# Performance work log

Hardware: AMD Instinct MI355X
Metric: run time of the kernel (lower is better)

## Reference

```python
import jax, jax.numpy as jnp
import numpy as np

DIM = 256      # in_channels == hidden_channels
INNER = 256    # heads * dim_head
HEADS = 4
DH = 64        # dim_head = hidden_channels // num_heads
EDGE_DIM = 512 # 2 * in_channels
FF = 1024      # 4 * dim ff expansion
DEPTH = 2
OUT = 1
N = 50000      # two stacked graphs of 25000 nodes
E = 100000
HALF = 25000


def setup_inputs() -> dict:
    key = jax.random.key(0)
    ks = iter(jax.random.split(key, 32))

    def lin(fan_in, fan_out):
        w = jax.random.normal(next(ks), (DEPTH, fan_in, fan_out), jnp.float32) * (1.0 / np.sqrt(fan_in))
        b = jnp.zeros((DEPTH, fan_out), jnp.float32)
        return w, b

    x = jax.random.normal(next(ks), (N, DIM), jnp.float32)
    edge_index = jax.random.randint(next(ks), (2, E), 0, HALF, dtype=jnp.int32)
    Wq, bq = lin(DIM, INNER)
    Wkv, bkv = lin(DIM, 2 * INNER)
    We, be = lin(EDGE_DIM, INNER)
    Wo, bo = lin(INNER, DIM)
    W1, b1 = lin(DIM, FF)
    W2, b2 = lin(FF, DIM)
    g_attn = jax.random.normal(next(ks), (DEPTH, 3 * DIM, 1), jnp.float32) * (1.0 / np.sqrt(3 * DIM))
    g_ff = jax.random.normal(next(ks), (DEPTH, 3 * DIM, 1), jnp.float32) * (1.0 / np.sqrt(3 * DIM))
    ln1_g = jnp.ones((DEPTH, DIM), jnp.float32); ln1_b = jnp.zeros((DEPTH, DIM), jnp.float32)
    ln2_g = jnp.ones((DEPTH, DIM), jnp.float32); ln2_b = jnp.zeros((DEPTH, DIM), jnp.float32)
    Wout = jax.random.normal(next(ks), (DIM, OUT), jnp.float32) * (1.0 / np.sqrt(DIM))
    bout = jnp.zeros((OUT,), jnp.float32)
    return dict(x=x, edge_index=edge_index, ln1_g=ln1_g, ln1_b=ln1_b, Wq=Wq, bq=bq,
                Wkv=Wkv, bkv=bkv, We=We, be=be, Wo=Wo, bo=bo, g_attn=g_attn,
                ln2_g=ln2_g, ln2_b=ln2_b, W1=W1, b1=b1, W2=W2, b2=b2, g_ff=g_ff,
                Wout=Wout, bout=bout)


def _layer_norm(x, g, b):
    mu = jnp.mean(x, axis=-1, keepdims=True)
    var = jnp.mean(jnp.square(x - mu), axis=-1, keepdims=True)
    return (x - mu) * jax.lax.rsqrt(var + 1e-5) * g + b


def _gated_residual(x, res, w):
    # gate = sigmoid(Linear_no_bias(cat(x, res, x - res)))
    gate = jax.nn.sigmoid(jnp.concatenate([x, res, x - res], axis=-1) @ w)  # [n,1]
    return x * gate + res * (1.0 - gate)


def _forward(x, edge_index, ln1_g, ln1_b, Wq, bq, Wkv, bkv, We, be, Wo, bo, g_attn,
             ln2_g, ln2_b, W1, b1, W2, b2, g_ff, Wout, bout):
    src, dst = edge_index[0], edge_index[1]
    # edge_attr = cat(x[src], x[dst]) as built in DeepGraphTransformer_mse.forward
    edge_attr = jnp.concatenate([x[src], x[dst]], axis=-1)  # [E, 2*DIM]
    nodes = x
    n = nodes.shape[0]
    scale = DH ** -0.5
    for l in range(DEPTH):
        xn = _layer_norm(nodes, ln1_g[l], ln1_b[l])
        q = xn @ Wq[l] + bq[l]                                   # [n, INNER]
        k, v = jnp.split(xn @ Wkv[l] + bkv[l], 2, axis=-1)       # [n, INNER] each
        e = edge_attr @ We[l] + be[l]                            # [E, INNER]
        qe = q[dst].reshape(-1, HEADS, DH)                       # [E,H,Dh]
        ke = (k[src] + e).reshape(-1, HEADS, DH)
        ve = (v[src] + e).reshape(-1, HEADS, DH)
        sim = jnp.einsum('ehd,ehd->eh', qe, ke) * scale          # [E,H]
        smax = jax.ops.segment_max(sim, dst, num_segments=n)     # [n,H] (-inf for empty)
        ez = jnp.exp(sim - smax[dst])
        denom = jax.ops.segment_sum(ez, dst, num_segments=n)
        attn = ez / denom[dst]                                   # softmax over incoming edges
        agg = jax.ops.segment_sum(attn[:, :, None] * ve, dst, num_segments=n)
        attn_out = agg.reshape(n, INNER) @ Wo[l] + bo[l]         # [n, DIM]
        nodes = _gated_residual(attn_out, nodes, g_attn[l])
        xn2 = _layer_norm(nodes, ln2_g[l], ln2_b[l])
        h = jax.nn.gelu(xn2 @ W1[l] + b1[l], approximate=False) @ W2[l] + b2[l]
        nodes = _gated_residual(h, nodes, g_ff[l])
    z = nodes @ Wout + bout                                      # [n, OUT]
    return z


def reference(x, edge_index, ln1_g, ln1_b, Wq, bq, Wkv, bkv, We, be, Wo, bo, g_attn,
              ln2_g, ln2_b, W1, b1, W2, b2, g_ff, Wout, bout):
    z = _forward(x, edge_index, ln1_g, ln1_b, Wq, bq, Wkv, bkv, We, be, Wo, bo, g_attn,
                 ln2_g, ln2_b, W1, b1, W2, b2, g_ff, Wout, bout)
    half = z.shape[0] // 2
    z_old, z_new = z[:half], z[half:]
    return (z_new.reshape(-1), z_old, z_new)
```

## Files before the change

kernel.cpp:

```cpp
#include <hip/hip_runtime.h>
#include <cmath>

#define N_NODES 50000
#define N_EDGES 100000
#define HALF_N  25000
#define DIM     256
#define NDEPTH  2
#define MAXDEG  64

#define WT_QKVE 0
#define WT_WO   393216
#define WT_W1   524288
#define WT_W2   786432
#define WT_LAYER 1048576

typedef __bf16 bf16;
typedef bf16 bf16x8 __attribute__((ext_vector_type(8)));
typedef bf16 bf16x4 __attribute__((ext_vector_type(4)));
typedef float f32x4 __attribute__((ext_vector_type(4)));

__device__ __forceinline__ void lds_barrier() {
  asm volatile("s_waitcnt lgkmcnt(0)" ::: "memory");
  __builtin_amdgcn_s_barrier();
  __builtin_amdgcn_sched_barrier(0);
}

__device__ __forceinline__ float wave_sum(float v) {
  v += __shfl_xor(v, 1);
  v += __shfl_xor(v, 2);
  v += __shfl_xor(v, 4);
  v += __shfl_xor(v, 8);
  v += __shfl_xor(v, 16);
  v += __shfl_xor(v, 32);
  return v;
}

__device__ __forceinline__ float fast_gelu(float v) {
  float ax = fabsf(v) * 0.70710678118654752f;
  float t = __builtin_amdgcn_rcpf(fmaf(0.3275911f, ax, 1.0f));
  float p = t * fmaf(t, fmaf(t, fmaf(t, fmaf(t, 1.061405429f, -1.453152027f),
                                     1.421413741f), -0.284496736f), 0.254829592f);
  float e = __expf(-ax * ax);
  float erfv = fmaf(-p, e, 1.0f);
  float ph = copysignf(erfv, v);
  return 0.5f * v * (1.0f + ph);
}

__global__ void ln0_kernel(const float* __restrict__ in, const float* __restrict__ g,
                           const float* __restrict__ b, bf16* __restrict__ A2) {
  int row = blockIdx.x * 4 + (threadIdx.x >> 6);
  if (row >= HALF_N) return;
  int lane = threadIdx.x & 63;
  float4 x = reinterpret_cast<const float4*>(in + (size_t)row * DIM)[lane];
  float mu = wave_sum(x.x + x.y + x.z + x.w) * (1.0f / DIM);
  float d0 = x.x - mu, d1 = x.y - mu, d2 = x.z - mu, d3 = x.w - mu;
  float var = wave_sum(d0*d0 + d1*d1 + d2*d2 + d3*d3) * (1.0f / DIM);
  float r = rsqrtf(var + 1e-5f);
  float4 gv = reinterpret_cast<const float4*>(g)[lane];
  float4 bv = reinterpret_cast<const float4*>(b)[lane];
  bf16x4 o;
  o[0] = (bf16)(d0 * r * gv.x + bv.x);
  o[1] = (bf16)(d1 * r * gv.y + bv.y);
  o[2] = (bf16)(d2 * r * gv.z + bv.z);
  o[3] = (bf16)(d3 * r * gv.w + bv.w);
  *reinterpret_cast<bf16x4*>(A2 + (size_t)row * 512 + lane * 4) = o;
}

template<int KK, int NJ>
__global__ __launch_bounds__(256, 2) void gemm_nloop(
    const bf16* __restrict__ A, const bf16* __restrict__ Wp,
    const float* __restrict__ bias, bf16* __restrict__ C, int M) {
  constexpr int STEPS = KK / 64;
  __shared__ bf16x8 As[KK * 8];
  __shared__ bf16 Cs[64 * 128];
  const int tid = threadIdx.x;
  const int lane = tid & 63, wv = tid >> 6;
  const int lm = lane & 15, kb = (lane >> 4) & 3;
  const int row0 = blockIdx.x * 64;
#pragma unroll
  for (int i = 0; i < KK / 32; ++i) {
    int idx = tid + i * 256;
    int row = idx & 63, k8 = idx >> 6;
    int rga = row0 + row; if (rga >= M) rga = M - 1;
    As[idx] = *reinterpret_cast<const bf16x8*>(A + (size_t)rga * KK + k8 * 8);
  }
  const bf16x8* wb = reinterpret_cast<const bf16x8*>(Wp) + kb * 128 + wv * 32 + lm;
  bf16x8 pfr[2];
#pragma unroll
  for (int ni = 0; ni < 2; ++ni) pfr[ni] = wb[ni * 16];
  lds_barrier();
  for (int jn = 0; jn < NJ; ++jn) {
    f32x4 acc[4][2] = {};
#pragma unroll
    for (int st = 0; st < STEPS; ++st) {
#pragma unroll
      for (int ks = 0; ks < 2; ++ks) {
        bf16x8 bfr[2], af[4];
        if (st == 0 && ks == 0) {
          bfr[0] = pfr[0]; bfr[1] = pfr[1];
        } else {
#pragma unroll
          for (int ni = 0; ni < 2; ++ni)
            bfr[ni] = wb[(size_t)jn * (KK * 16) + st * 1024 + ks * 512 + ni * 16];
        }
#pragma unroll
        for (int mi = 0; mi < 4; ++mi)
          af[mi] = As[(st * 8 + ks * 4 + kb) * 64 + mi * 16 + lm];
#pragma unroll
        for (int mi = 0; mi < 4; ++mi)
#pragma unroll
          for (int ni = 0; ni < 2; ++ni)
            acc[mi][ni] = __builtin_amdgcn_mfma_f32_16x16x32_bf16(af[mi], bfr[ni], acc[mi][ni], 0, 0, 0);
      }
    }
    if (jn + 1 < NJ) {
#pragma unroll
      for (int ni = 0; ni < 2; ++ni)
        pfr[ni] = wb[(size_t)(jn + 1) * (KK * 16) + ni * 16];
    }
    lds_barrier();
#pragma unroll
    for (int ni = 0; ni < 2; ++ni) {
      int c = wv * 32 + ni * 16 + lm;
      float bval = bias[jn * 128 + c];
#pragma unroll
      for (int mi = 0; mi < 4; ++mi)
#pragma unroll
        for (int e = 0; e < 4; ++e) {
          int r = mi * 16 + kb * 4 + e;
          Cs[r * 128 + c] = (bf16)(acc[mi][ni][e] + bval);
        }
    }
    lds_barrier();
    bf16x8* C8 = reinterpret_cast<bf16x8*>(C);
    const bf16x8* Cs8 = (const bf16x8*)Cs;
#pragma unroll
    for (int i = 0; i < 4; ++i) {
      int idx = tid + i * 256;
      int row = idx >> 4, c8 = idx & 15;
      int grow = row0 + row;
      if (grow < M) C8[(size_t)grow * (NJ * 16) + jn * 16 + c8] = Cs8[row * 16 + c8];
    }
  }
}

__global__ __launch_bounds__(256, 2) void wo_fused(
    const bf16* __restrict__ agg, const bf16* __restrict__ A2,
    const bf16* __restrict__ Wp, const float* __restrict__ bvec,
    const float* __restrict__ bo, const int* __restrict__ deg,
    const float* __restrict__ gattn, const float* __restrict__ ln2g,
    const float* __restrict__ ln2b, float* __restrict__ nodes,
    bf16* __restrict__ xn, int rows) {
  __shared__ bf16x8 As[2048];
  __shared__ bf16 Cs[64 * 256];
  const int tid = threadIdx.x;
  const int lane = tid & 63, wv = tid >> 6;
  const int row0 = blockIdx.x * 64;
  if (row0 < HALF_N) {
    const int wr = wv >> 1, wc = wv & 1;
    const int lm = lane & 15, kb = (lane >> 4) & 3;
#pragma unroll
    for (int i = 0; i < 8; ++i) {
      int idx = tid + i * 256;
      int row = idx & 63, k8 = idx >> 6;
      int rga = row0 + row; if (rga >= HALF_N) rga = HALF_N - 1;
      As[idx] = *reinterpret_cast<const bf16x8*>(agg + (size_t)rga * 256 + k8 * 8);
    }
    bf16x8 afx[2][8];
#pragma unroll
    for (int mi = 0; mi < 2; ++mi) {
      int row = row0 + wr * 32 + mi * 16 + lm;
      if (row >= HALF_N) row = HALF_N - 1;
      const bf16* pa = A2 + (size_t)row * 512 + 256 + kb * 8;
#pragma unroll
      for (int t = 0; t < 8; ++t)
        afx[mi][t] = *reinterpret_cast<const bf16x8*>(pa + t * 32);
    }
    lds_barrier();
    const bf16x8* wb = reinterpret_cast<const bf16x8*>(Wp) + kb * 128 + wc * 64 + lm;
    for (int jn = 0; jn < 2; ++jn) {
      f32x4 acc[2][4] = {};
#pragma unroll
      for (int st = 0; st < 8; ++st) {
#pragma unroll
        for (int ks = 0; ks < 2; ++ks) {
          bf16x8 bfr[4], af[2];
#pragma unroll
          for (int ni = 0; ni < 4; ++ni)
            bfr[ni] = wb[jn * 8192 + (st * 8 + ks * 4) * 128 + ni * 16];
#pragma unroll
          for (int mi = 0; mi < 2; ++mi)
            af[mi] = (st < 4) ? As[(st * 8 + ks * 4 + kb) * 64 + wr * 32 + mi * 16 + lm]
                              : afx[mi][(st - 4) * 2 + ks];
#pragma unroll
          for (int mi = 0; mi < 2; ++mi)
#pragma unroll
            for (int ni = 0; ni < 4; ++ni)
              acc[mi][ni] = __builtin_amdgcn_mfma_f32_16x16x32_bf16(af[mi], bfr[ni], acc[mi][ni], 0, 0, 0);
        }
      }
#pragma unroll
      for (int ni = 0; ni < 4; ++ni) {
        int cfull = jn * 128 + wc * 64 + ni * 16 + lm;
        float bval = bvec[cfull];
#pragma unroll
        for (int mi = 0; mi < 2; ++mi)
#pragma unroll
          for (int e = 0; e < 4; ++e) {
            int r = wr * 32 + mi * 16 + kb * 4 + e;
            int ch = (cfull >> 3) ^ (r & 7);
            Cs[r * 256 + ch * 8 + (cfull & 7)] = (bf16)(acc[mi][ni][e] + bval);
          }
      }
    }
    lds_barrier();
    for (int pass = 0; pass < 16; ++pass) {
      int r = pass * 4 + wv;
      int grow = row0 + r;
      float x0, x1, x2, x3;
      if (grow >= HALF_N || deg[grow] == 0) {
        float4 bo4 = reinterpret_cast<const float4*>(bo)[lane];
        x0 = bo4.x; x1 = bo4.y; x2 = bo4.z; x3 = bo4.w;
      } else {
        int ch = (lane >> 1) ^ (r & 7);
        bf16x4 c4 = *reinterpret_cast<const bf16x4*>(Cs + r * 256 + ch * 8 + (lane & 1) * 4);
        x0 = (float)c4[0]; x1 = (float)c4[1]; x2 = (float)c4[2]; x3 = (float)c4[3];
      }
      float4 rv = reinterpret_cast<const float4*>(nodes + (size_t)grow * 256)[lane];
      float4 w0 = reinterpret_cast<const float4*>(gattn)[lane];
      float4 w1 = reinterpret_cast<const float4*>(gattn + 256)[lane];
      float4 w2 = reinterpret_cast<const float4*>(gattn + 512)[lane];
      float dot = x0 * (w0.x + w2.x) + rv.x * (w1.x - w2.x)
                + x1 * (w0.y + w2.y) + rv.y * (w1.y - w2.y)
                + x2 * (w0.z + w2.z) + rv.z * (w1.z - w2.z)
                + x3 * (w0.w + w2.w) + rv.w * (w1.w - w2.w);
      dot = wave_sum(dot);
      float gate = 1.0f / (1.0f + __expf(-dot));
      float n0 = fmaf(x0 - rv.x, gate, rv.x);
      float n1 = fmaf(x1 - rv.y, gate, rv.y);
      float n2 = fmaf(x2 - rv.z, gate, rv.z);
      float n3 = fmaf(x3 - rv.w, gate, rv.w);
      float4 o; o.x = n0; o.y = n1; o.z = n2; o.w = n3;
      reinterpret_cast<float4*>(nodes + (size_t)grow * 256)[lane] = o;
      float mu = wave_sum(n0 + n1 + n2 + n3) * (1.0f / DIM);
      float d0 = n0 - mu, d1 = n1 - mu, d2 = n2 - mu, d3 = n3 - mu;
      float var = wave_sum(d0*d0 + d1*d1 + d2*d2 + d3*d3) * (1.0f / DIM);
      float rs = rsqrtf(var + 1e-5f);
      float4 gv = reinterpret_cast<const float4*>(ln2g)[lane];
      float4 bv = reinterpret_cast<const float4*>(ln2b)[lane];
      bf16x4 ob;
      ob[0] = (bf16)(d0 * rs * gv.x + bv.x);
      ob[1] = (bf16)(d1 * rs * gv.y + bv.y);
      ob[2] = (bf16)(d2 * rs * gv.z + bv.z);
      ob[3] = (bf16)(d3 * rs * gv.w + bv.w);
      *reinterpret_cast<bf16x4*>(xn + (size_t)grow * 256 + lane * 4) = ob;
    }
  } else {
    float4 bo4 = reinterpret_cast<const float4*>(bo)[lane];
    for (int pass = 0; pass < 16; ++pass) {
      int grow = row0 + pass * 4 + wv;
      if (grow >= rows) continue;
      float x0 = bo4.x, x1 = bo4.y, x2 = bo4.z, x3 = bo4.w;
      float4 rv = reinterpret_cast<const float4*>(nodes + (size_t)grow * 256)[lane];
      float4 w0 = reinterpret_cast<const float4*>(gattn)[lane];
      float4 w1 = reinterpret_cast<const float4*>(gattn + 256)[lane];
      float4 w2 = reinterpret_cast<const float4*>(gattn + 512)[lane];
      float dot = x0 * (w0.x + w2.x) + rv.x * (w1.x - w2.x)
                + x1 * (w0.y + w2.y) + rv.y * (w1.y - w2.y)
                + x2 * (w0.z + w2.z) + rv.z * (w1.z - w2.z)
                + x3 * (w0.w + w2.w) + rv.w * (w1.w - w2.w);
      dot = wave_sum(dot);
      float gate = 1.0f / (1.0f + __expf(-dot));
      float n0 = fmaf(x0 - rv.x, gate, rv.x);
      float n1 = fmaf(x1 - rv.y, gate, rv.y);
      float n2 = fmaf(x2 - rv.z, gate, rv.z);
      float n3 = fmaf(x3 - rv.w, gate, rv.w);
      float4 o; o.x = n0; o.y = n1; o.z = n2; o.w = n3;
      reinterpret_cast<float4*>(nodes + (size_t)grow * 256)[lane] = o;
      float mu = wave_sum(n0 + n1 + n2 + n3) * (1.0f / DIM);
      float d0 = n0 - mu, d1 = n1 - mu, d2 = n2 - mu, d3 = n3 - mu;
      float var = wave_sum(d0*d0 + d1*d1 + d2*d2 + d3*d3) * (1.0f / DIM);
      float rs = rsqrtf(var + 1e-5f);
      float4 gv = reinterpret_cast<const float4*>(ln2g)[lane];
      float4 bv = reinterpret_cast<const float4*>(ln2b)[lane];
      bf16x4 ob;
      ob[0] = (bf16)(d0 * rs * gv.x + bv.x);
      ob[1] = (bf16)(d1 * rs * gv.y + bv.y);
      ob[2] = (bf16)(d2 * rs * gv.z + bv.z);
      ob[3] = (bf16)(d3 * rs * gv.w + bv.w);
      *reinterpret_cast<bf16x4*>(xn + (size_t)grow * 256 + lane * 4) = ob;
    }
  }
}

template<int LAST>
__global__ __launch_bounds__(512, 4) void ff_fused(
    const bf16* __restrict__ A, const bf16* __restrict__ W1p,
    const float* __restrict__ b1, const bf16* __restrict__ W2p,
    const float* __restrict__ b2, float* __restrict__ nodes,
    const float* __restrict__ gff, const float* __restrict__ ln1g,
    const float* __restrict__ ln1b, bf16* __restrict__ A2,
    const float* __restrict__ Wout, const float* __restrict__ bout,
    float* __restrict__ out, int M) {
  __shared__ char smem[65536];
  bf16x8* Xs = (bf16x8*)smem;
  bf16*   Cs = (bf16*)smem;
  bf16x8* Hs = (bf16x8*)(smem + 32768);
  const int tid = threadIdx.x;
  const int lane = tid & 63, wv = tid >> 6;
  const int lm = lane & 15, kb = (lane >> 4) & 3;
  const int row0 = blockIdx.x * 64;
#pragma unroll
  for (int i = 0; i < 4; ++i) {
    int idx = tid + i * 512;
    int row = idx & 63, k8 = idx >> 6;
    int rga = row0 + row; if (rga >= M) rga = M - 1;
    Xs[idx] = *reinterpret_cast<const bf16x8*>(A + (size_t)rga * 256 + k8 * 8);
  }
  lds_barrier();
  const bf16x8* w1b = (const bf16x8*)W1p + kb * 128 + wv * 16 + lm;
  const bf16x8* w2b = (const bf16x8*)W2p + kb * 256 + wv * 32 + lm;
  f32x4 acc[4][2] = {};
  for (int j = 0; j < 8; ++j) {
    bf16x8 pf2[4];
#pragma unroll
    for (int ks = 0; ks < 2; ++ks)
#pragma unroll
      for (int ni = 0; ni < 2; ++ni)
        pf2[ks * 2 + ni] = w2b[j * 4096 + ks * 1024 + ni * 16];
    f32x4 acc1[4] = {};
#pragma unroll
    for (int half = 0; half < 2; ++half) {
#pragma unroll
      for (int ks = 0; ks < 4; ++ks) {
        bf16x8 bfr = w1b[j * 4096 + half * 2048 + ks * 512];
        bf16x8 af[4];
#pragma unroll
        for (int mi = 0; mi < 4; ++mi)
          af[mi] = Xs[(half * 16 + ks * 4 + kb) * 64 + mi * 16 + lm];
#pragma unroll
        for (int mi = 0; mi < 4; ++mi)
          acc1[mi] = __builtin_amdgcn_mfma_f32_16x16x32_bf16(af[mi], bfr, acc1[mi], 0, 0, 0);
      }
    }
    {
      bf16* hsb = (bf16*)(Hs + (j & 1) * 1024);
      int c = wv * 16 + lm;
      float bval = b1[j * 128 + c];
#pragma unroll
      for (int mi = 0; mi < 4; ++mi)
#pragma unroll
        for (int e = 0; e < 4; ++e) {
          int r = mi * 16 + kb * 4 + e;
          float v = fast_gelu(acc1[mi][e] + bval);
          hsb[((c >> 3) * 64 + r) * 8 + (c & 7)] = (bf16)v;
        }
    }
    lds_barrier();
    const bf16x8* hb = Hs + (j & 1) * 1024;
#pragma unroll
    for (int h2 = 0; h2 < 2; ++h2) {
#pragma unroll
      for (int ks = 0; ks < 2; ++ks) {
        bf16x8 bfr[2], af[4];
#pragma unroll
        for (int ni = 0; ni < 2; ++ni)
          bfr[ni] = (h2 == 0) ? pf2[ks * 2 + ni]
                              : w2b[j * 4096 + 2048 + ks * 1024 + ni * 16];
#pragma unroll
        for (int mi = 0; mi < 4; ++mi)
          af[mi] = hb[(h2 * 8 + ks * 4 + kb) * 64 + mi * 16 + lm];
#pragma unroll
        for (int mi = 0; mi < 4; ++mi)
#pragma unroll
          for (int ni = 0; ni < 2; ++ni)
            acc[mi][ni] = __builtin_amdgcn_mfma_f32_16x16x32_bf16(af[mi], bfr[ni], acc[mi][ni], 0, 0, 0);
      }
    }
  }
#pragma unroll
  for (int ni = 0; ni < 2; ++ni) {
    int c = wv * 32 + ni * 16 + lm;
    float bval = b2[c];
#pragma unroll
    for (int mi = 0; mi < 4; ++mi)
#pragma unroll
      for (int e = 0; e < 4; ++e) {
        int r = mi * 16 + kb * 4 + e;
        int ch = (c >> 3) ^ (r & 7);
        Cs[r * 256 + ch * 8 + (c & 7)] = (bf16)(acc[mi][ni][e] + bval);
      }
  }
  lds_barrier();
  for (int pass = 0; pass < 8; ++pass) {
    int r = pass * 8 + wv;
    int grow = row0 + r;
    if (grow >= M) continue;
    int ch = (lane >> 1) ^ (r & 7);
    bf16x4 c4 = *reinterpret_cast<const bf16x4*>(Cs + r * 256 + ch * 8 + (lane & 1) * 4);
    float x0 = (float)c4[0], x1 = (float)c4[1], x2 = (float)c4[2], x3 = (float)c4[3];
    float4 rv = reinterpret_cast<const float4*>(nodes + (size_t)grow * 256)[lane];
    float4 w0 = reinterpret_cast<const float4*>(gff)[lane];
    float4 w1 = reinterpret_cast<const float4*>(gff + 256)[lane];
    float4 w2 = reinterpret_cast<const float4*>(gff + 512)[lane];
    float dot = x0 * (w0.x + w2.x) + rv.x * (w1.x - w2.x)
              + x1 * (w0.y + w2.y) + rv.y * (w1.y - w2.y)
              + x2 * (w0.z + w2.z) + rv.z * (w1.z - w2.z)
              + x3 * (w0.w + w2.w) + rv.w * (w1.w - w2.w);
    dot = wave_sum(dot);
    float gate = 1.0f / (1.0f + __expf(-dot));
    float n0 = fmaf(x0 - rv.x, gate, rv.x);
    float n1 = fmaf(x1 - rv.y, gate, rv.y);
    float n2 = fmaf(x2 - rv.z, gate, rv.z);
    float n3 = fmaf(x3 - rv.w, gate, rv.w);
    if (LAST) {
      float4 wo4 = reinterpret_cast<const float4*>(Wout)[lane];
      float z = n0 * wo4.x + n1 * wo4.y + n2 * wo4.z + n3 * wo4.w;
      z = wave_sum(z);
      if (lane == 0) {
        z += bout[0];
        if (grow < HALF_N) {
          out[HALF_N + grow] = z;
        } else {
          int jj = grow - HALF_N;
          out[jj] = z;
          out[2 * HALF_N + jj] = z;
        }
      }
    } else {
      float4 o; o.x = n0; o.y = n1; o.z = n2; o.w = n3;
      reinterpret_cast<float4*>(nodes + (size_t)grow * 256)[lane] = o;
      if (grow < HALF_N) {
        float mu = wave_sum(n0 + n1 + n2 + n3) * (1.0f / DIM);
        float d0 = n0 - mu, d1 = n1 - mu, d2 = n2 - mu, d3 = n3 - mu;
        float var = wave_sum(d0*d0 + d1*d1 + d2*d2 + d3*d3) * (1.0f / DIM);
        float rs = rsqrtf(var + 1e-5f);
        float4 gv = reinterpret_cast<const float4*>(ln1g)[lane];
        float4 bv = reinterpret_cast<const float4*>(ln1b)[lane];
        bf16x4 ob;
        ob[0] = (bf16)(d0 * rs * gv.x + bv.x);
        ob[1] = (bf16)(d1 * rs * gv.y + bv.y);
        ob[2] = (bf16)(d2 * rs * gv.z + bv.z);
        ob[3] = (bf16)(d3 * rs * gv.w + bv.w);
        *reinterpret_cast<bf16x4*>(A2 + (size_t)grow * 512 + lane * 4) = ob;
      }
    }
  }
}

__global__ void ell_build(const int* __restrict__ ei, int* __restrict__ deg,
                          int* __restrict__ ell) {
  int e = blockIdx.x * 256 + threadIdx.x;
  if (e >= N_EDGES) return;
  int s = ei[e], d = ei[N_EDGES + e];
  int pos = atomicAdd(&deg[d], 1);
  if (pos < MAXDEG) ell[d * MAXDEG + pos] = s;
}

__global__ void attn_gather(const int* __restrict__ deg, const int* __restrict__ ell,
                            const bf16* __restrict__ qkv, bf16* __restrict__ agg) {
  int d = blockIdx.x * 4 + (threadIdx.x >> 6);
  if (d >= HALF_N) return;
  int lane = threadIdx.x & 63;
  int cnt = deg[d]; if (cnt > MAXDEG) cnt = MAXDEG;
  const bf16* qr = qkv + (size_t)d * 768;
  bf16x4 qb = *reinterpret_cast<const bf16x4*>(qr + lane * 4);
  float q0 = (float)qb[0], q1 = (float)qb[1], q2 = (float)qb[2], q3 = (float)qb[3];
  float m = -INFINITY, den = 0.0f, a0 = 0.0f, a1 = 0.0f, a2 = 0.0f, a3 = 0.0f;
  int i = 0;
  for (; i + 2 <= cnt; i += 2) {
    int s0 = ell[d * MAXDEG + i];
    int s1 = ell[d * MAXDEG + i + 1];
    bf16x8 k0 = *reinterpret_cast<const bf16x8*>(qkv + (size_t)s0 * 768 + 256 + lane * 8);
    bf16x8 k1 = *reinterpret_cast<const bf16x8*>(qkv + (size_t)s1 * 768 + 256 + lane * 8);
    float p0 = q0 * (float)k0[0] + q1 * (float)k0[1] + q2 * (float)k0[2] + q3 * (float)k0[3];
    float p1 = q0 * (float)k1[0] + q1 * (float)k1[1] + q2 * (float)k1[2] + q3 * (float)k1[3];
    p0 += __shfl_xor(p0, 1); p1 += __shfl_xor(p1, 1);
    p0 += __shfl_xor(p0, 2); p1 += __shfl_xor(p1, 2);
    p0 += __shfl_xor(p0, 4); p1 += __shfl_xor(p1, 4);
    p0 += __shfl_xor(p0, 8); p1 += __shfl_xor(p1, 8);
    float s0v = p0 * 0.125f, s1v = p1 * 0.125f;
    float nm = fmaxf(m, fmaxf(s0v, s1v));
    float sc = __expf(m - nm);
    float w0 = __expf(s0v - nm), w1 = __expf(s1v - nm);
    den = den * sc + w0 + w1;
    a0 = a0 * sc + w0 * (float)k0[4] + w1 * (float)k1[4];
    a1 = a1 * sc + w0 * (float)k0[5] + w1 * (float)k1[5];
    a2 = a2 * sc + w0 * (float)k0[6] + w1 * (float)k1[6];
    a3 = a3 * sc + w0 * (float)k0[7] + w1 * (float)k1[7];
    m = nm;
  }
  if (i < cnt) {
    int s = ell[d * MAXDEG + i];
    bf16x8 kv8 = *reinterpret_cast<const bf16x8*>(qkv + (size_t)s * 768 + 256 + lane * 8);
    float p = q0 * (float)kv8[0] + q1 * (float)kv8[1] + q2 * (float)kv8[2] + q3 * (float)kv8[3];
    p += __shfl_xor(p, 1); p += __shfl_xor(p, 2);
    p += __shfl_xor(p, 4); p += __shfl_xor(p, 8);
    float sim = p * 0.125f;
    float nm = fmaxf(m, sim);
    float sc = __expf(m - nm);
    float w = __expf(sim - nm);
    den = den * sc + w;
    a0 = a0 * sc + w * (float)kv8[4];
    a1 = a1 * sc + w * (float)kv8[5];
    a2 = a2 * sc + w * (float)kv8[6];
    a3 = a3 * sc + w * (float)kv8[7];
    m = nm;
  }
  bf16x4 o;
  if (cnt > 0) {
    float inv = 1.0f / den;
    o[0] = (bf16)(a0 * inv);
    o[1] = (bf16)(a1 * inv);
    o[2] = (bf16)(a2 * inv);
    o[3] = (bf16)(a3 * inv);
  } else {
    o[0] = (bf16)0.0f; o[1] = (bf16)0.0f; o[2] = (bf16)0.0f; o[3] = (bf16)0.0f;
  }
  *reinterpret_cast<bf16x4*>(agg + (size_t)d * DIM + lane * 4) = o;
}

__global__ void prep_w(const float* __restrict__ Wq, const float* __restrict__ Wkv,
                       const float* __restrict__ We, const float* __restrict__ Wo,
                       const float* __restrict__ W1, const float* __restrict__ W2,
                       bf16* __restrict__ wt) {
  int idx = blockIdx.x * 256 + threadIdx.x;
  if (idx >= 2 * WT_LAYER) return;
  int l = idx / WT_LAYER, r = idx % WT_LAYER;
  float v;
  if (r < 393216) {
    int jn = r >> 16, t = r & 65535;
    int k8 = t >> 10, u = t & 1023, n = u >> 3, e = u & 7;
    int ncol = jn * 128 + n, k = k8 * 8 + e;
    if (ncol < 256) {
      v = (k < 256) ? Wq[l * 65536 + k * 256 + ncol] : 0.0f;
    } else {
      int u2 = ncol - 256;
      int c = (u2 >> 3) * 4 + (u2 & 3);
      int half = (u2 >> 2) & 1;
      if (k < 256) v = Wkv[l * 131072 + k * 512 + half * 256 + c];
      else         v = We[l * 131072 + (k - 256) * 256 + c];
    }
  } else if (r < 524288) {
    int rr = r - 393216;
    int jn = rr >> 16, t = rr & 65535;
    int k8 = t >> 10, u = t & 1023, n = u >> 3, e = u & 7;
    int k = k8 * 8 + e;
    if (k >= 256) return;
    v = Wo[l * 65536 + k * 256 + jn * 128 + n];
  } else if (r < 786432) {
    int rr = r - 524288;
    int j = rr >> 15, t = rr & 32767;
    int k8 = t >> 10, u = t & 1023, n = u >> 3, e = u & 7;
    v = W1[l * 262144 + (k8 * 8 + e) * 1024 + j * 128 + n];
  } else {
    int rr = r - 786432;
    int j = rr >> 15, t = rr & 32767;
    int k8 = t >> 11, u = t & 2047, n = u >> 3, e = u & 7;
    v = W2[l * 262144 + (j * 128 + k8 * 8 + e) * 256 + n];
  }
  wt[idx] = (bf16)v;
}

__global__ void prep_weff(const float* __restrict__ We, const float* __restrict__ Wo,
                          bf16* __restrict__ wt) {
  int idx = blockIdx.x * 256 + threadIdx.x;
  if (idx >= 2 * 65536) return;
  int l = idx >> 16, r = idx & 65535;
  int k = r >> 8, n = r & 255;
  const float* wer = We + l * 131072 + (256 + k) * 256;
  const float* wor = Wo + l * 65536 + n;
  float acc = 0.0f;
#pragma unroll 4
  for (int m = 0; m < 256; ++m) acc += wer[m] * wor[m * 256];
  int kf = 256 + k;
  size_t off = (size_t)l * WT_LAYER + WT_WO +
               (n >> 7) * 65536 + (kf >> 3) * 1024 + (n & 127) * 8 + (kf & 7);
  wt[off] = (bf16)acc;
}

__global__ void prep_bvec(const float* __restrict__ be, const float* __restrict__ Wo,
                          const float* __restrict__ bo, float* __restrict__ biasq) {
  int idx = blockIdx.x * 256 + threadIdx.x;
  if (idx >= 512) return;
  int l = idx >> 8, n = idx & 255;
  const float* ber = be + l * 256;
  const float* wor = Wo + l * 65536 + n;
  float acc = bo[l * 256 + n];
#pragma unroll 4
  for (int m = 0; m < 256; ++m) acc += ber[m] * wor[m * 256];
  biasq[1536 + l * 256 + n] = acc;
}

__global__ void prep_bias(const float* __restrict__ bq, const float* __restrict__ bkv,
                          float* __restrict__ biasq) {
  int i = blockIdx.x * 256 + threadIdx.x;
  if (i >= 1536) return;
  int l = i / 768, n = i % 768;
  float v;
  if (n < 256) v = bq[l * 256 + n];
  else {
    int u2 = n - 256;
    int c = (u2 >> 3) * 4 + (u2 & 3);
    int half = (u2 >> 2) & 1;
    v = bkv[l * 512 + half * 256 + c];
  }
  biasq[i] = v;
}

__global__ void prep_x(const float* __restrict__ x, bf16* __restrict__ A2) {
  int i = blockIdx.x * 256 + threadIdx.x;
  if (i >= HALF_N * 64) return;
  int row = i >> 6, c = i & 63;
  float4 v = reinterpret_cast<const float4*>(x)[i];
  bf16x4 o;
  o[0] = (bf16)v.x; o[1] = (bf16)v.y; o[2] = (bf16)v.z; o[3] = (bf16)v.w;
  *reinterpret_cast<bf16x4*>(A2 + (size_t)row * 512 + 256 + c * 4) = o;
}

extern "C" void kernel_launch(void* const* d_in, const int* in_sizes, int n_in,
                              void* d_out, int out_size, void* d_ws, size_t ws_size,
                              hipStream_t stream) {
  const float* x     = (const float*)d_in[0];
  const int*   ei    = (const int*)d_in[1];
  const float* ln1_g = (const float*)d_in[2];
  const float* ln1_b = (const float*)d_in[3];
  const float* Wq    = (const float*)d_in[4];
  const float* bq    = (const float*)d_in[5];
  const float* Wkv   = (const float*)d_in[6];
  const float* bkv   = (const float*)d_in[7];
  const float* We    = (const float*)d_in[8];
  const float* be    = (const float*)d_in[9];
  const float* Wo    = (const float*)d_in[10];
  const float* bo    = (const float*)d_in[11];
  const float* g_attn= (const float*)d_in[12];
  const float* ln2_g = (const float*)d_in[13];
  const float* ln2_b = (const float*)d_in[14];
  const float* W1    = (const float*)d_in[15];
  const float* b1    = (const float*)d_in[16];
  const float* W2    = (const float*)d_in[17];
  const float* b2    = (const float*)d_in[18];
  const float* g_ff  = (const float*)d_in[19];
  const float* Wout  = (const float*)d_in[20];
  const float* bout  = (const float*)d_in[21];
  float* out = (float*)d_out;

  char* base = (char*)d_ws;
  float* nodes   = (float*)base;  base += (size_t)N_NODES * DIM * 4;
  bf16*  A2      = (bf16*)base;   base += (size_t)HALF_N * 512 * 2;
  bf16*  xn_bf   = (bf16*)base;   base += (size_t)N_NODES * DIM * 2;
  bf16*  qkv     = (bf16*)base;   base += (size_t)HALF_N * 768 * 2;
  bf16*  agg     = (bf16*)base;   base += (size_t)HALF_N * DIM * 2;
  bf16*  wt      = (bf16*)base;   base += (size_t)2 * WT_LAYER * 2;
  float* biasq   = (float*)base;  base += 2048 * 4;
  int*   deg     = (int*)base;    base += HALF_N * 4;
  int*   ell     = (int*)base;    base += (size_t)HALF_N * MAXDEG * 4;

  hipMemcpyAsync(nodes, x, (size_t)N_NODES * DIM * sizeof(float),
                 hipMemcpyDeviceToDevice, stream);
  prep_w<<<(2 * WT_LAYER + 255) / 256, 256, 0, stream>>>(Wq, Wkv, We, Wo, W1, W2, wt);
  prep_weff<<<(2 * 65536 + 255) / 256, 256, 0, stream>>>(We, Wo, wt);
  prep_bvec<<<2, 256, 0, stream>>>(be, Wo, bo, biasq);
  prep_bias<<<6, 256, 0, stream>>>(bq, bkv, biasq);
  prep_x<<<(HALF_N * 64 + 255) / 256, 256, 0, stream>>>(x, A2);
  hipMemsetAsync(deg, 0, HALF_N * sizeof(int), stream);
  ell_build<<<(N_EDGES + 255) / 256, 256, 0, stream>>>(ei, deg, ell);

  const int GP_H = (HALF_N + 63) / 64;
  const int GP_N = (N_NODES + 63) / 64;

  for (int l = 0; l < NDEPTH; ++l) {
    const bf16* wl = wt + (size_t)l * WT_LAYER;
    if (l == 0)
      ln0_kernel<<<(HALF_N + 3) / 4, 256, 0, stream>>>(x, ln1_g, ln1_b, A2);
    gemm_nloop<512, 6><<<GP_H, 256, 0, stream>>>(A2, wl + WT_QKVE, biasq + l * 768, qkv, HALF_N);
    attn_gather<<<(HALF_N + 3) / 4, 256, 0, stream>>>(deg, ell, qkv, agg);
    wo_fused<<<GP_N, 256, 0, stream>>>(agg, A2, wl + WT_WO, biasq + 1536 + l * 256,
                                       bo + l * DIM, deg, g_attn + l * 768,
                                       ln2_g + l * DIM, ln2_b + l * DIM,
                                       nodes, xn_bf, N_NODES);
    if (l < NDEPTH - 1) {
      ff_fused<0><<<GP_N, 512, 0, stream>>>(
          xn_bf, wl + WT_W1, b1 + l * 1024, wl + WT_W2, b2 + l * DIM,
          nodes, g_ff + l * 768, ln1_g + (l + 1) * DIM, ln1_b + (l + 1) * DIM, A2,
          nullptr, nullptr, nullptr, N_NODES);
    } else {
      ff_fused<1><<<GP_N, 512, 0, stream>>>(
          xn_bf, wl + WT_W1, b1 + l * 1024, wl + WT_W2, b2 + l * DIM,
          nodes, g_ff + l * 768, nullptr, nullptr, nullptr,
          Wout, bout, out, N_NODES);
    }
  }
}
```

Before: 499.7 us.

## Approximate GELU with exp2 sigmoid, widen QKV GEMM to 512 threads, hoist params

Replaces the erf-polynomial GELU with a cheaper sigmoid-form approximation based on one exp2 and one reciprocal. The QKV GEMM block is doubled to 8 waves, each computing a single 16-column tile, for more parallelism per block. Gate weights, LayerNorm parameters and Wout are loaded once per thread, outside the row loops, in the fused kernels. The GELU approximation changes numerics relative to exact erf GELU and may affect accuracy.

```diff
diff --git a/kernel.cpp b/kernel.cpp
--- a/kernel.cpp
+++ b/kernel.cpp
@@ -35,15 +35,11 @@
   return v;
 }
 
-__device__ __forceinline__ float fast_gelu(float v) {
-  float ax = fabsf(v) * 0.70710678118654752f;
-  float t = __builtin_amdgcn_rcpf(fmaf(0.3275911f, ax, 1.0f));
-  float p = t * fmaf(t, fmaf(t, fmaf(t, fmaf(t, 1.061405429f, -1.453152027f),
-                                     1.421413741f), -0.284496736f), 0.254829592f);
-  float e = __expf(-ax * ax);
-  float erfv = fmaf(-p, e, 1.0f);
-  float ph = copysignf(erfv, v);
-  return 0.5f * v * (1.0f + ph);
+__device__ __forceinline__ float fast_gelu(float x) {
+  float p = x * x;
+  float q = fmaf(p, -0.10294437f, -2.3022112f);
+  float e = exp2f(x * q);
+  return x * __builtin_amdgcn_rcpf(1.0f + e);
 }
 
 __global__ void ln0_kernel(const float* __restrict__ in, const float* __restrict__ g,
@@ -67,7 +63,7 @@
 }
 
 template<int KK, int NJ>
-__global__ __launch_bounds__(256, 2) void gemm_nloop(
+__global__ __launch_bounds__(512, 2) void gemm_nloop(
     const bf16* __restrict__ A, const bf16* __restrict__ Wp,
     const float* __restrict__ bias, bf16* __restrict__ C, int M) {
   constexpr int STEPS = KK / 64;
@@ -78,65 +74,52 @@
   const int lm = lane & 15, kb = (lane >> 4) & 3;
   const int row0 = blockIdx.x * 64;
 #pragma unroll
-  for (int i = 0; i < KK / 32; ++i) {
-    int idx = tid + i * 256;
+  for (int i = 0; i < KK / 64; ++i) {
+    int idx = tid + i * 512;
     int row = idx & 63, k8 = idx >> 6;
     int rga = row0 + row; if (rga >= M) rga = M - 1;
     As[idx] = *reinterpret_cast<const bf16x8*>(A + (size_t)rga * KK + k8 * 8);
   }
-  const bf16x8* wb = reinterpret_cast<const bf16x8*>(Wp) + kb * 128 + wv * 32 + lm;
-  bf16x8 pfr[2];
-#pragma unroll
-  for (int ni = 0; ni < 2; ++ni) pfr[ni] = wb[ni * 16];
+  const bf16x8* wb = reinterpret_cast<const bf16x8*>(Wp) + kb * 128 + wv * 16 + lm;
+  bf16x8 pfr = wb[0];
   lds_barrier();
   for (int jn = 0; jn < NJ; ++jn) {
-    f32x4 acc[4][2] = {};
+    f32x4 acc[4] = {};
 #pragma unroll
     for (int st = 0; st < STEPS; ++st) {
 #pragma unroll
       for (int ks = 0; ks < 2; ++ks) {
-        bf16x8 bfr[2], af[4];
-        if (st == 0 && ks == 0) {
-          bfr[0] = pfr[0]; bfr[1] = pfr[1];
-        } else {
-#pragma unroll
-          for (int ni = 0; ni < 2; ++ni)
-            bfr[ni] = wb[(size_t)jn * (KK * 16) + st * 1024 + ks * 512 + ni * 16];
-        }
+        bf16x8 bfr = (st == 0 && ks == 0)
+                   ? pfr
+                   : wb[(size_t)jn * (KK * 16) + st * 1024 + ks * 512];
+        bf16x8 af[4];
 #pragma unroll
         for (int mi = 0; mi < 4; ++mi)
           af[mi] = As[(st * 8 + ks * 4 + kb) * 64 + mi * 16 + lm];
 #pragma unroll
         for (int mi = 0; mi < 4; ++mi)
-#pragma unroll
-          for (int ni = 0; ni < 2; ++ni)
-            acc[mi][ni] = __builtin_amdgcn_mfma_f32_16x16x32_bf16(af[mi], bfr[ni], acc[mi][ni], 0, 0, 0);
-      }
-    }
-    if (jn + 1 < NJ) {
-#pragma unroll
-      for (int ni = 0; ni < 2; ++ni)
-        pfr[ni] = wb[(size_t)(jn + 1) * (KK * 16) + ni * 16];
-    }
+          acc[mi] = __builtin_amdgcn_mfma_f32_16x16x32_bf16(af[mi], bfr, acc[mi], 0, 0, 0);
+      }
+    }
+    if (jn + 1 < NJ) pfr = wb[(size_t)(jn + 1) * (KK * 16)];
     lds_barrier();
-#pragma unroll
-    for (int ni = 0; ni < 2; ++ni) {
-      int c = wv * 32 + ni * 16 + lm;
+    {
+      int c = wv * 16 + lm;
       float bval = bias[jn * 128 + c];
 #pragma unroll
       for (int mi = 0; mi < 4; ++mi)
 #pragma unroll
         for (int e = 0; e < 4; ++e) {
           int r = mi * 16 + kb * 4 + e;
-          Cs[r * 128 + c] = (bf16)(acc[mi][ni][e] + bval);
+          Cs[r * 128 + c] = (bf16)(acc[mi][e] + bval);
         }
     }
     lds_barrier();
     bf16x8* C8 = reinterpret_cast<bf16x8*>(C);
     const bf16x8* Cs8 = (const bf16x8*)Cs;
 #pragma unroll
-    for (int i = 0; i < 4; ++i) {
-      int idx = tid + i * 256;
+    for (int i = 0; i < 2; ++i) {
+      int idx = tid + i * 512;
       int row = idx >> 4, c8 = idx & 15;
       int grow = row0 + row;
       if (grow < M) C8[(size_t)grow * (NJ * 16) + jn * 16 + c8] = Cs8[row * 16 + c8];
@@ -156,6 +139,14 @@
   const int tid = threadIdx.x;
   const int lane = tid & 63, wv = tid >> 6;
   const int row0 = blockIdx.x * 64;
+  float4 w0 = reinterpret_cast<const float4*>(gattn)[lane];
+  float4 w1 = reinterpret_cast<const float4*>(gattn + 256)[lane];
+  float4 w2 = reinterpret_cast<const float4*>(gattn + 512)[lane];
+  float4 wa, wbv;
+  wa.x = w0.x + w2.x; wa.y = w0.y + w2.y; wa.z = w0.z + w2.z; wa.w = w0.w + w2.w;
+  wbv.x = w1.x - w2.x; wbv.y = w1.y - w2.y; wbv.z = w1.z - w2.z; wbv.w = w1.w - w2.w;
+  float4 gv = reinterpret_cast<const float4*>(ln2g)[lane];
+  float4 bv = reinterpret_cast<const float4*>(ln2b)[lane];
   if (row0 < HALF_N) {
     const int wr = wv >> 1, wc = wv & 1;
     const int lm = lane & 15, kb = (lane >> 4) & 3;
@@ -227,13 +218,8 @@
         x0 = (float)c4[0]; x1 = (float)c4[1]; x2 = (float)c4[2]; x3 = (float)c4[3];
       }
       float4 rv = reinterpret_cast<const float4*>(nodes + (size_t)grow * 256)[lane];
-      float4 w0 = reinterpret_cast<const float4*>(gattn)[lane];
-      float4 w1 = reinterpret_cast<const float4*>(gattn + 256)[lane];
-      float4 w2 = reinterpret_cast<const float4*>(gattn + 512)[lane];
-      float dot = x0 * (w0.x + w2.x) + rv.x * (w1.x - w2.x)
-                + x1 * (w0.y + w2.y) + rv.y * (w1.y - w2.y)
-                + x2 * (w0.z + w2.z) + rv.z * (w1.z - w2.z)
-                + x3 * (w0.w + w2.w) + rv.w * (w1.w - w2.w);
+      float dot = x0 * wa.x + rv.x * wbv.x + x1 * wa.y + rv.y * wbv.y
+                + x2 * wa.z + rv.z * wbv.z + x3 * wa.w + rv.w * wbv.w;
       dot = wave_sum(dot);
       float gate = 1.0f / (1.0f + __expf(-dot));
       float n0 = fmaf(x0 - rv.x, gate, rv.x);
@@ -246,8 +232,6 @@
       float d0 = n0 - mu, d1 = n1 - mu, d2 = n2 - mu, d3 = n3 - mu;
       float var = wave_sum(d0*d0 + d1*d1 + d2*d2 + d3*d3) * (1.0f / DIM);
       float rs = rsqrtf(var + 1e-5f);
-      float4 gv = reinterpret_cast<const float4*>(ln2g)[lane];
-      float4 bv = reinterpret_cast<const float4*>(ln2b)[lane];
       bf16x4 ob;
       ob[0] = (bf16)(d0 * rs * gv.x + bv.x);
       ob[1] = (bf16)(d1 * rs * gv.y + bv.y);
@@ -262,13 +246,8 @@
       if (grow >= rows) continue;
       float x0 = bo4.x, x1 = bo4.y, x2 = bo4.z, x3 = bo4.w;
       float4 rv = reinterpret_cast<const float4*>(nodes + (size_t)grow * 256)[lane];
-      float4 w0 = reinterpret_cast<const float4*>(gattn)[lane];
-      float4 w1 = reinterpret_cast<const float4*>(gattn + 256)[lane];
-      float4 w2 = reinterpret_cast<const float4*>(gattn + 512)[lane];
-      float dot = x0 * (w0.x + w2.x) + rv.x * (w1.x - w2.x)
-                + x1 * (w0.y + w2.y) + rv.y * (w1.y - w2.y)
-                + x2 * (w0.z + w2.z) + rv.z * (w1.z - w2.z)
-                + x3 * (w0.w + w2.w) + rv.w * (w1.w - w2.w);
+      float dot = x0 * wa.x + rv.x * wbv.x + x1 * wa.y + rv.y * wbv.y
+                + x2 * wa.z + rv.z * wbv.z + x3 * wa.w + rv.w * wbv.w;
       dot = wave_sum(dot);
       float gate = 1.0f / (1.0f + __expf(-dot));
       float n0 = fmaf(x0 - rv.x, gate, rv.x);
@@ -281,8 +260,6 @@
       float d0 = n0 - mu, d1 = n1 - mu, d2 = n2 - mu, d3 = n3 - mu;
       float var = wave_sum(d0*d0 + d1*d1 + d2*d2 + d3*d3) * (1.0f / DIM);
       float rs = rsqrtf(var + 1e-5f);
-      float4 gv = reinterpret_cast<const float4*>(ln2g)[lane];
-      float4 bv = reinterpret_cast<const float4*>(ln2b)[lane];
       bf16x4 ob;
       ob[0] = (bf16)(d0 * rs * gv.x + bv.x);
       ob[1] = (bf16)(d1 * rs * gv.y + bv.y);
@@ -391,6 +368,19 @@
         Cs[r * 256 + ch * 8 + (c & 7)] = (bf16)(acc[mi][ni][e] + bval);
       }
   }
+  float4 w0 = reinterpret_cast<const float4*>(gff)[lane];
+  float4 w1 = reinterpret_cast<const float4*>(gff + 256)[lane];
+  float4 w2 = reinterpret_cast<const float4*>(gff + 512)[lane];
+  float4 wa, wbv;
+  wa.x = w0.x + w2.x; wa.y = w0.y + w2.y; wa.z = w0.z + w2.z; wa.w = w0.w + w2.w;
+  wbv.x = w1.x - w2.x; wbv.y = w1.y - w2.y; wbv.z = w1.z - w2.z; wbv.w = w1.w - w2.w;
+  float4 gv, bv, wo4;
+  if (LAST) {
+    wo4 = reinterpret_cast<const float4*>(Wout)[lane];
+  } else {
+    gv = reinterpret_cast<const float4*>(ln1g)[lane];
+    bv = reinterpret_cast<const float4*>(ln1b)[lane];
+  }
   lds_barrier();
   for (int pass = 0; pass < 8; ++pass) {
     int r = pass * 8 + wv;
@@ -400,13 +390,8 @@
     bf16x4 c4 = *reinterpret_cast<const bf16x4*>(Cs + r * 256 + ch * 8 + (lane & 1) * 4);
     float x0 = (float)c4[0], x1 = (float)c4[1], x2 = (float)c4[2], x3 = (float)c4[3];
     float4 rv = reinterpret_cast<const float4*>(nodes + (size_t)grow * 256)[lane];
-    float4 w0 = reinterpret_cast<const float4*>(gff)[lane];
-    float4 w1 = reinterpret_cast<const float4*>(gff + 256)[lane];
-    float4 w2 = reinterpret_cast<const float4*>(gff + 512)[lane];
-    float dot = x0 * (w0.x + w2.x) + rv.x * (w1.x - w2.x)
-              + x1 * (w0.y + w2.y) + rv.y * (w1.y - w2.y)
-              + x2 * (w0.z + w2.z) + rv.z * (w1.z - w2.z)
-              + x3 * (w0.w + w2.w) + rv.w * (w1.w - w2.w);
+    float dot = x0 * wa.x + rv.x * wbv.x + x1 * wa.y + rv.y * wbv.y
+              + x2 * wa.z + rv.z * wbv.z + x3 * wa.w + rv.w * wbv.w;
     dot = wave_sum(dot);
     float gate = 1.0f / (1.0f + __expf(-dot));
     float n0 = fmaf(x0 - rv.x, gate, rv.x);
@@ -414,7 +399,6 @@
     float n2 = fmaf(x2 - rv.z, gate, rv.z);
     float n3 = fmaf(x3 - rv.w, gate, rv.w);
     if (LAST) {
-      float4 wo4 = reinterpret_cast<const float4*>(Wout)[lane];
       float z = n0 * wo4.x + n1 * wo4.y + n2 * wo4.z + n3 * wo4.w;
       z = wave_sum(z);
       if (lane == 0) {
@@ -435,8 +419,6 @@
         float d0 = n0 - mu, d1 = n1 - mu, d2 = n2 - mu, d3 = n3 - mu;
         float var = wave_sum(d0*d0 + d1*d1 + d2*d2 + d3*d3) * (1.0f / DIM);
         float rs = rsqrtf(var + 1e-5f);
-        float4 gv = reinterpret_cast<const float4*>(ln1g)[lane];
-        float4 bv = reinterpret_cast<const float4*>(ln1b)[lane];
         bf16x4 ob;
         ob[0] = (bf16)(d0 * rs * gv.x + bv.x);
         ob[1] = (bf16)(d1 * rs * gv.y + bv.y);
@@ -673,7 +655,7 @@
     const bf16* wl = wt + (size_t)l * WT_LAYER;
     if (l == 0)
       ln0_kernel<<<(HALF_N + 3) / 4, 256, 0, stream>>>(x, ln1_g, ln1_b, A2);
-    gemm_nloop<512, 6><<<GP_H, 256, 0, stream>>>(A2, wl + WT_QKVE, biasq + l * 768, qkv, HALF_N);
+    gemm_nloop<512, 6><<<GP_H, 512, 0, stream>>>(A2, wl + WT_QKVE, biasq + l * 768, qkv, HALF_N);
     attn_gather<<<(HALF_N + 3) / 4, 256, 0, stream>>>(deg, ell, qkv, agg);
     wo_fused<<<GP_N, 256, 0, stream>>>(agg, A2, wl + WT_WO, biasq + 1536 + l * 256,
                                        bo + l * DIM, deg, g_attn + l * 768,
```

Result: faster. 468.2 us (-6.3%).
